# Kernel tuning notes

Hardware: AMD Instinct MI355X
Metric: run time of the kernel (lower is better)

The kernel has to match this reference:

```python
import jax, jax.numpy as jnp
import numpy as np

B, C_IN, S = 32, 4, 2048
NF = 256          # CNN filters
H = 256           # LSTM hidden per direction
NH, DH = 8, 64    # heads, single-head size
MH = 512          # multihead size
KSZ, PAD, POOL = 13, 6, 6
SP = (S + 2 * PAD - KSZ + 1) // POOL  # 341: post conv(len-preserving)+maxpool1d length


def _lstm_dir(x, Wih, Whh, b):
    # x: [T, N, C] -- torch LSTM gate order i,f,g,o; b = b_ih + b_hh merged
    N = x.shape[1]
    h0 = jnp.zeros((N, H), x.dtype)
    c0 = jnp.zeros((N, H), x.dtype)

    def step(carry, xt):
        h, c = carry
        g = xt @ Wih.T + h @ Whh.T + b
        i, f, gg, o = jnp.split(g, 4, axis=-1)
        c = jax.nn.sigmoid(f) * c + jax.nn.sigmoid(i) * jnp.tanh(gg)
        h = jax.nn.sigmoid(o) * jnp.tanh(c)
        return (h, c), h

    _, hs = jax.lax.scan(step, (h0, c0), x)
    return hs


def _bilstm(x, Wih, Whh, b):
    fwd = _lstm_dir(x, Wih[0], Whh[0], b[0])
    bwd = _lstm_dir(x[::-1], Wih[1], Whh[1], b[1])[::-1]
    return jnp.concatenate([fwd, bwd], axis=-1)


def _rpe():
    # RelativePosition: |clip(k-q, -(S-1), S-1)| / (S-1); identical across the
    # batch-repeat channels, so compute once then broadcast (same math).
    r = jnp.arange(S)
    d = jnp.abs(jnp.clip(r[None, :] - r[:, None], -(S - 1), S - 1))
    d = d.astype(jnp.float32) / jnp.float32(S - 1)
    # nn.MaxPool2d((9,9), stride=(6,6), padding=1) -> [341, 341]
    return jax.lax.reduce_window(d, -jnp.inf, jax.lax.max, (9, 9), (6, 6), [(1, 1), (1, 1)])


def setup_inputs():
    key = jax.random.key(0)
    ks = jax.random.split(key, 20)
    f = lambda i, shape: jax.random.normal(ks[i], shape, jnp.float32) * 0.05
    return {
        "inputs": jax.random.normal(ks[0], (B, C_IN, S), jnp.float32),
        "conv1_w": f(1, (NF, C_IN, KSZ)),
        "bn1_gamma": jnp.ones((NF,), jnp.float32),
        "bn1_beta": jnp.zeros((NF,), jnp.float32),
        "Wih0": f(2, (2, 4 * H, NF)),
        "Whh0": f(3, (2, 4 * H, H)),
        "b0": f(4, (2, 4 * H)),
        "Wih1": f(5, (2, 4 * H, 2 * H)),
        "Whh1": f(6, (2, 4 * H, H)),
        "b1": f(7, (2, 4 * H)),
        "Qw": f(8, (NH, DH, 2 * H)), "Qb": f(9, (NH, DH)),
        "Kw": f(10, (NH, DH, 2 * H)), "Kb": f(11, (NH, DH)),
        "Vw": f(12, (NH, DH, 2 * H)), "Vb": f(13, (NH, DH)),
        "mh_w": f(14, (MH, NH * DH)), "mh_b": f(15, (MH,)),
    }


def reference(inputs, conv1_w, bn1_gamma, bn1_beta, Wih0, Whh0, b0,
              Wih1, Whh1, b1, Qw, Qb, Kw, Kb, Vw, Vb, mh_w, mh_b):
    # layer1: Conv1d (bias=False, pad=6 keeps length) + BatchNorm1d(eval: mean=0, var=1) + ReLU + MaxPool1d(6)
    x = jax.lax.conv_general_dilated(inputs, conv1_w, (1,), [(PAD, PAD)],
                                     dimension_numbers=('NCH', 'OIH', 'NCH'))
    x = x * (bn1_gamma / jnp.sqrt(1.0 + 1e-5))[None, :, None] + bn1_beta[None, :, None]
    x = jax.nn.relu(x)
    x = jax.lax.reduce_window(x, -jnp.inf, jax.lax.max, (1, 1, POOL), (1, 1, POOL), 'VALID')  # [B,NF,SP]
    x = jnp.transpose(x, (0, 2, 1))  # [B, SP, NF]

    # torch nn.LSTM with batch_first=False fed [B,SP,NF]: scans over axis 0 (batch) -- replicated faithfully.
    x = _bilstm(x, Wih0, Whh0, b0)
    x = _bilstm(x, Wih1, Whh1, b1)  # [B, SP, 2H]
    # (the F_RNN/R_RNN split-and-concat is an identity)

    # per-head Q/K/V (batched over heads), relative attention, dropout off (eval)
    q = jnp.einsum('bsc,hdc->hbsd', x, Qw) + Qb[:, None, None, :]
    k = jnp.einsum('bsc,hdc->hbsd', x, Kw) + Kb[:, None, None, :]
    v = jnp.einsum('bsc,hdc->hbsd', x, Vw) + Vb[:, None, None, :]
    scores = jnp.einsum('hbqd,hbkd->hbqk', q, k) / jnp.sqrt(jnp.float32(DH))
    scores = scores / _rpe()[None, None, :, :]
    p = jax.nn.softmax(scores, axis=-1)
    attn = jax.nn.relu(jnp.einsum('hbqk,hbkd->hbqd', p, v))  # [NH,B,SP,DH]
    cat = jnp.transpose(attn, (1, 2, 0, 3)).reshape(B, SP, NH * DH)
    out = jax.nn.relu(cat @ mh_w.T + mh_b)  # MultiHeadLinear + MHReLU
    return out
```

## Files before the change

### kernel.cpp

```cpp
#include <hip/hip_runtime.h>
#include <math.h>

#define B_    32
#define CIN   4
#define SLEN  2048
#define NF    256
#define HD    256
#define SP    341
#define RTOT  (B_*SP)
#define NH_   8
#define DH_   64
#define GRP   4
#define PSTR  344
#define HS    (SP*HD)
#define PKS   768

typedef __attribute__((ext_vector_type(8))) short short8;
typedef __attribute__((ext_vector_type(4))) float floatx4;
typedef __attribute__((ext_vector_type(4))) unsigned short ushortx4;
typedef __attribute__((ext_vector_type(8))) unsigned short ushort8;

__device__ __forceinline__ float sigmoidf_(float x) { return 1.0f / (1.0f + expf(-x)); }

__device__ __forceinline__ unsigned short f2bf(float x) {
    unsigned int u = __float_as_uint(x);
    unsigned int r = (u + 0x7FFF + ((u >> 16) & 1)) >> 16;
    return (unsigned short)r;
}
__device__ __forceinline__ float bf2f(unsigned short b) {
    return __uint_as_float(((unsigned int)b) << 16);
}

__device__ __forceinline__ void store_f4_llc(float* p, floatx4 v)
{
    asm volatile("global_store_dwordx4 %0, %1, off sc0 sc1" :: "v"(p), "v"(v) : "memory");
}
__device__ __forceinline__ unsigned load_u32_llc(const unsigned* p)
{
    unsigned r;
    asm volatile("global_load_dword %0, %1, off sc0 sc1\n\ts_waitcnt vmcnt(0)"
                 : "=v"(r) : "v"(p) : "memory");
    return r;
}
__device__ __forceinline__ void load_h16_llc(const float* p, floatx4* r)
{
    asm volatile(
        "global_load_dwordx4 %0, %16, off sc0 sc1\n\t"
        "global_load_dwordx4 %1, %16, off offset:16 sc0 sc1\n\t"
        "global_load_dwordx4 %2, %16, off offset:128 sc0 sc1\n\t"
        "global_load_dwordx4 %3, %16, off offset:144 sc0 sc1\n\t"
        "global_load_dwordx4 %4, %16, off offset:256 sc0 sc1\n\t"
        "global_load_dwordx4 %5, %16, off offset:272 sc0 sc1\n\t"
        "global_load_dwordx4 %6, %16, off offset:384 sc0 sc1\n\t"
        "global_load_dwordx4 %7, %16, off offset:400 sc0 sc1\n\t"
        "global_load_dwordx4 %8, %16, off offset:512 sc0 sc1\n\t"
        "global_load_dwordx4 %9, %16, off offset:528 sc0 sc1\n\t"
        "global_load_dwordx4 %10, %16, off offset:640 sc0 sc1\n\t"
        "global_load_dwordx4 %11, %16, off offset:656 sc0 sc1\n\t"
        "global_load_dwordx4 %12, %16, off offset:768 sc0 sc1\n\t"
        "global_load_dwordx4 %13, %16, off offset:784 sc0 sc1\n\t"
        "global_load_dwordx4 %14, %16, off offset:896 sc0 sc1\n\t"
        "global_load_dwordx4 %15, %16, off offset:912 sc0 sc1\n\t"
        "s_waitcnt vmcnt(0)"
        : "=&v"(r[0]), "=&v"(r[1]), "=&v"(r[2]), "=&v"(r[3]),
          "=&v"(r[4]), "=&v"(r[5]), "=&v"(r[6]), "=&v"(r[7]),
          "=&v"(r[8]), "=&v"(r[9]), "=&v"(r[10]), "=&v"(r[11]),
          "=&v"(r[12]), "=&v"(r[13]), "=&v"(r[14]), "=&v"(r[15])
        : "v"(p)
        : "memory");
}


__global__ __launch_bounds__(256)
void conv_pool_k(const float* __restrict__ in, const float* __restrict__ cw,
                 const float* __restrict__ gamma, const float* __restrict__ beta,
                 unsigned short* __restrict__ x0p)
{
    const int b  = blockIdx.y;
    const int s0 = blockIdx.x * 16;
    const int co = threadIdx.x;
    __shared__ float ins[CIN][16*6 + 12];
    for (int idx = threadIdx.x; idx < CIN*108; idx += 256) {
        int ci = idx / 108, o = idx % 108;
        int pos = 6*s0 - 6 + o;
        ins[ci][o] = (pos >= 0 && pos < SLEN) ? in[(b*CIN + ci)*SLEN + pos] : 0.0f;
    }
    float wreg[52];
    {
        const float4* wp = (const float4*)(cw + co*52);
        #pragma unroll
        for (int j4 = 0; j4 < 13; ++j4) {
            float4 w4 = wp[j4];
            wreg[j4*4+0]=w4.x; wreg[j4*4+1]=w4.y; wreg[j4*4+2]=w4.z; wreg[j4*4+3]=w4.w;
        }
    }
    const float scale = gamma[co] * (1.0f / sqrtf(1.0f + 1e-5f));
    const float shift = beta[co];
    __syncthreads();
    for (int si = 0; si < 16; ++si) {
        int s = s0 + si;
        if (s >= SP) break;
        float win[CIN][18];
        #pragma unroll
        for (int ci = 0; ci < CIN; ++ci)
            #pragma unroll
            for (int o = 0; o < 18; ++o)
                win[ci][o] = ins[ci][6*si + o];
        float m = -1e30f;
        #pragma unroll
        for (int p6 = 0; p6 < 6; ++p6) {
            float acc = 0.0f;
            #pragma unroll
            for (int ci = 0; ci < CIN; ++ci)
                #pragma unroll
                for (int kk = 0; kk < 13; ++kk)
                    acc += win[ci][p6+kk] * wreg[ci*13+kk];
            float val = acc * scale + shift;
            val = fmaxf(val, 0.0f);
            m = fmaxf(m, val);
        }
        unsigned short hb_ = f2bf(m);
        unsigned short lb_ = f2bf(m - bf2f(hb_));
        size_t rb = (size_t)(b*SP + s)*512 + (size_t)(co >> 3)*16 + (co & 7);
        x0p[rb]     = hb_;
        x0p[rb + 8] = lb_;
    }
}

__global__ __launch_bounds__(256)
void pack4_k(const float* __restrict__ W, unsigned short* __restrict__ hi,
             unsigned short* __restrict__ lo, int n4)
{
    int i = blockIdx.x * 256 + threadIdx.x;
    if (i >= n4) return;
    float4 x = *((const float4*)W + i);
    float v[4] = {x.x, x.y, x.z, x.w};
    ushortx4 h, l;
    #pragma unroll
    for (int e = 0; e < 4; ++e) {
        unsigned short hb = f2bf(v[e]);
        h[e] = hb;
        l[e] = f2bf(v[e] - bf2f(hb));
    }
    *((ushortx4*)hi + i) = h;
    *((ushortx4*)lo + i) = l;
}

__global__ __launch_bounds__(256)
void pack8_k(const float* __restrict__ W, unsigned short* __restrict__ O, int n8)
{
    int i = blockIdx.x * 256 + threadIdx.x;
    if (i >= n8) return;
    const float4* wp = (const float4*)W + (size_t)i*2;
    float4 a = wp[0], b = wp[1];
    float v[8] = {a.x,a.y,a.z,a.w,b.x,b.y,b.z,b.w};
    ushort8 h, l;
    #pragma unroll
    for (int e = 0; e < 8; ++e) {
        unsigned short hb = f2bf(v[e]);
        h[e] = hb;
        l[e] = f2bf(v[e] - bf2f(hb));
    }
    *(ushort8*)(O + (size_t)i*16)     = h;
    *(ushort8*)(O + (size_t)i*16 + 8) = l;
}

template<int RELU>
__global__ __launch_bounds__(256)
void gemm_bf_k(const unsigned short* __restrict__ Ap, const unsigned short* __restrict__ Bp,
               const float* __restrict__ bias, float* __restrict__ C,
               int M, int N, int K)
{
    const int n0 = blockIdx.x * 128;
    const int m0 = blockIdx.y * 128;
    const int tid = threadIdx.x;
    const int lane = tid & 63;
    const int w = tid >> 6;
    const int wm = w >> 1, wn = w & 1;
    const int ln15 = lane & 15, lq = lane >> 4;
    const int l8 = lane >> 3, lj = lane & 7;
    const size_t rstr = 2*(size_t)K;

    __shared__ unsigned short As[128*64];
    __shared__ unsigned short Bs[128*64];

    floatx4 acc[4][4];
    #pragma unroll
    for (int i = 0; i < 4; ++i)
        #pragma unroll
        for (int j = 0; j < 4; ++j) acc[i][j] = (floatx4){0.f, 0.f, 0.f, 0.f};

    int rloc[4];
    #pragma unroll
    for (int c = 0; c < 4; ++c) rloc[c] = w*32 + c*8 + l8;
    const int spos = lj ^ (l8 & 7);

    for (int k0 = 0; k0 < K; k0 += 32) {
        short8 va[4], vb[4];
        #pragma unroll
        for (int c = 0; c < 4; ++c) {
            int gra = m0 + rloc[c]; if (gra >= M) gra = M - 1;
            va[c] = *(const short8*)(Ap + (size_t)gra*rstr + k0*2 + lj*8);
            vb[c] = *(const short8*)(Bp + (size_t)(n0 + rloc[c])*rstr + k0*2 + lj*8);
        }
        __syncthreads();
        #pragma unroll
        for (int c = 0; c < 4; ++c) {
            *(short8*)&As[rloc[c]*64 + spos*8] = va[c];
            *(short8*)&Bs[rloc[c]*64 + spos*8] = vb[c];
        }
        __syncthreads();

        short8 fa_h[4], fa_l[4], fb_h[4], fb_l[4];
        #pragma unroll
        for (int mt = 0; mt < 4; ++mt) {
            const int lr = wm*64 + mt*16 + ln15;
            fa_h[mt] = *(const short8*)&As[lr*64 + (((lq*2  ) ^ (lr&7))*8)];
            fa_l[mt] = *(const short8*)&As[lr*64 + (((lq*2+1) ^ (lr&7))*8)];
        }
        #pragma unroll
        for (int nt = 0; nt < 4; ++nt) {
            const int lr = wn*64 + nt*16 + ln15;
            fb_h[nt] = *(const short8*)&Bs[lr*64 + (((lq*2  ) ^ (lr&7))*8)];
            fb_l[nt] = *(const short8*)&Bs[lr*64 + (((lq*2+1) ^ (lr&7))*8)];
        }
        #pragma unroll
        for (int mt = 0; mt < 4; ++mt)
            #pragma unroll
            for (int nt = 0; nt < 4; ++nt) {
                acc[mt][nt] = __builtin_amdgcn_mfma_f32_16x16x32_bf16(fa_l[mt], fb_h[nt], acc[mt][nt], 0, 0, 0);
                acc[mt][nt] = __builtin_amdgcn_mfma_f32_16x16x32_bf16(fa_h[mt], fb_l[nt], acc[mt][nt], 0, 0, 0);
                acc[mt][nt] = __builtin_amdgcn_mfma_f32_16x16x32_bf16(fa_h[mt], fb_h[nt], acc[mt][nt], 0, 0, 0);
            }
    }

    #pragma unroll
    for (int nt = 0; nt < 4; ++nt) {
        const int n = n0 + wn*64 + nt*16 + ln15;
        const float bv = bias[n];
        #pragma unroll
        for (int mt = 0; mt < 4; ++mt) {
            const int mbase = m0 + wm*64 + mt*16 + lq*4;
            #pragma unroll
            for (int r = 0; r < 4; ++r) {
                int m = mbase + r;
                if (m < M) {
                    float val = acc[mt][nt][r] + bv;
                    if (RELU) val = fmaxf(val, 0.0f);
                    C[(size_t)m*N + n] = val;
                }
            }
        }
    }
}

__global__ __launch_bounds__(256)
void gemm_vT_k(const unsigned short* __restrict__ Ap, const unsigned short* __restrict__ Bp,
               const float* __restrict__ bias, unsigned short* __restrict__ vT,
               int M, int N, int K)
{
    const int n0 = blockIdx.x * 128;
    const int m0 = blockIdx.y * 128;
    const int tid = threadIdx.x;
    const int lane = tid & 63;
    const int w = tid >> 6;
    const int wm = w >> 1, wn = w & 1;
    const int ln15 = lane & 15, lq = lane >> 4;
    const int l8 = lane >> 3, lj = lane & 7;
    const size_t rstr = 2*(size_t)K;

    __shared__ unsigned short As[128*64];
    __shared__ unsigned short Bs[128*64];

    floatx4 acc[4][4];
    #pragma unroll
    for (int i = 0; i < 4; ++i)
        #pragma unroll
        for (int j = 0; j < 4; ++j) acc[i][j] = (floatx4){0.f, 0.f, 0.f, 0.f};

    int rloc[4];
    #pragma unroll
    for (int c = 0; c < 4; ++c) rloc[c] = w*32 + c*8 + l8;
    const int spos = lj ^ (l8 & 7);

    for (int k0 = 0; k0 < K; k0 += 32) {
        short8 va[4], vb[4];
        #pragma unroll
        for (int c = 0; c < 4; ++c) {
            int gra = m0 + rloc[c]; if (gra >= M) gra = M - 1;
            va[c] = *(const short8*)(Ap + (size_t)gra*rstr + k0*2 + lj*8);
            vb[c] = *(const short8*)(Bp + (size_t)(n0 + rloc[c])*rstr + k0*2 + lj*8);
        }
        __syncthreads();
        #pragma unroll
        for (int c = 0; c < 4; ++c) {
            *(short8*)&As[rloc[c]*64 + spos*8] = va[c];
            *(short8*)&Bs[rloc[c]*64 + spos*8] = vb[c];
        }
        __syncthreads();

        short8 fa_h[4], fa_l[4], fb_h[4], fb_l[4];
        #pragma unroll
        for (int mt = 0; mt < 4; ++mt) {
            const int lr = wm*64 + mt*16 + ln15;
            fa_h[mt] = *(const short8*)&As[lr*64 + (((lq*2  ) ^ (lr&7))*8)];
            fa_l[mt] = *(const short8*)&As[lr*64 + (((lq*2+1) ^ (lr&7))*8)];
        }
        #pragma unroll
        for (int nt = 0; nt < 4; ++nt) {
            const int lr = wn*64 + nt*16 + ln15;
            fb_h[nt] = *(const short8*)&Bs[lr*64 + (((lq*2  ) ^ (lr&7))*8)];
            fb_l[nt] = *(const short8*)&Bs[lr*64 + (((lq*2+1) ^ (lr&7))*8)];
        }
        #pragma unroll
        for (int mt = 0; mt < 4; ++mt)
            #pragma unroll
            for (int nt = 0; nt < 4; ++nt) {
                acc[mt][nt] = __builtin_amdgcn_mfma_f32_16x16x32_bf16(fa_l[mt], fb_h[nt], acc[mt][nt], 0, 0, 0);
                acc[mt][nt] = __builtin_amdgcn_mfma_f32_16x16x32_bf16(fa_h[mt], fb_l[nt], acc[mt][nt], 0, 0, 0);
                acc[mt][nt] = __builtin_amdgcn_mfma_f32_16x16x32_bf16(fa_h[mt], fb_h[nt], acc[mt][nt], 0, 0, 0);
            }
    }

    #pragma unroll
    for (int nt = 0; nt < 4; ++nt) {
        const int n = n0 + wn*64 + nt*16 + ln15;
        const float bv = bias[n];
        #pragma unroll
        for (int mt = 0; mt < 4; ++mt) {
            const int mbase = m0 + wm*64 + mt*16 + lq*4;
            #pragma unroll
            for (int r = 0; r < 4; ++r) {
                int m = mbase + r;
                if (m < M) {
                    float val = acc[mt][nt][r] + bv;
                    int bg = m / 341;
                    int sp = m - bg*341;
                    size_t vb_ = ((size_t)bg*512 + n)*PKS + (size_t)((sp >> 3)*16 + (sp & 7));
                    unsigned short hb16 = f2bf(val);
                    vT[vb_]     = hb16;
                    vT[vb_ + 8] = f2bf(val - bf2f(hb16));
                }
            }
        }
    }
}

__global__ __launch_bounds__(256)
void lstm_scan_k(const float* __restrict__ G,
                 const unsigned short* __restrict__ Whi,
                 const unsigned short* __restrict__ Wlo,
                 float* __restrict__ hb,
                 unsigned short* __restrict__ x_out,
                 unsigned* __restrict__ bar)
{
    const int j0 = blockIdx.x * 32;
    const int m0 = blockIdx.y * 32;
    const int d  = blockIdx.z;
    const int tid = threadIdx.x;
    const int w = tid >> 6, lane = tid & 63;
    const int mhalf = w & 1, gpair = w >> 1;
    const int ln15 = lane & 15, lq = lane >> 4;
    const size_t hsz = (size_t)2*SP*HD;
    unsigned* gbar = bar + (size_t)(blockIdx.y*2 + blockIdx.z)*64;

    __shared__ float Csh[32][132];

    int am = m0 + mhalf*16 + ln15; if (am > SP-1) am = SP-1;
    const int akoff = lq * 8;

    const unsigned short* WhiD = Whi + (size_t)d*1024*256;
    const unsigned short* WloD = Wlo + (size_t)d*1024*256;
    int nrow[4];
    #pragma unroll
    for (int t = 0; t < 4; ++t)
        nrow[t] = (gpair*2 + (t>>1))*256 + j0 + (t&1)*16 + ln15;

    const int emloc = tid >> 3;
    const int ej4   = (tid & 7) * 4;
    const int em    = m0 + emloc;

    floatx4 creg = (floatx4){0.f, 0.f, 0.f, 0.f};

    for (int s = 0; s < B_; ++s) {
        const int t_in = d ? (B_ - 1 - s) : s;
        float* hbuf_in  = hb + (size_t)(s & 1)*hsz;
        float* hbuf_out = hb + (size_t)((s+1) & 1)*hsz;

        floatx4 acc[4];
        #pragma unroll
        for (int t = 0; t < 4; ++t) acc[t] = (floatx4){0.f, 0.f, 0.f, 0.f};

        if (s > 0) {
            const float* p = hbuf_in + (size_t)d*HS + (size_t)am*HD + akoff;
            floatx4 hr[16];
            load_h16_llc(p, hr);
            #pragma unroll
            for (int kk = 0; kk < 8; ++kk) {
                const int ko = kk*32 + akoff;
                float vv[8] = {hr[2*kk][0], hr[2*kk][1], hr[2*kk][2], hr[2*kk][3],
                               hr[2*kk+1][0], hr[2*kk+1][1], hr[2*kk+1][2], hr[2*kk+1][3]};
                short8 ahi, alo;
                #pragma unroll
                for (int e = 0; e < 8; ++e) {
                    unsigned short hb16 = f2bf(vv[e]);
                    ahi[e] = (short)hb16;
                    alo[e] = (short)f2bf(vv[e] - bf2f(hb16));
                }
                #pragma unroll
                for (int t = 0; t < 4; ++t) {
                    short8 bhi = *(const short8*)(WhiD + (size_t)nrow[t]*HD + ko);
                    short8 blo = *(const short8*)(WloD + (size_t)nrow[t]*HD + ko);
                    acc[t] = __builtin_amdgcn_mfma_f32_16x16x32_bf16(alo, bhi, acc[t], 0, 0, 0);
                    acc[t] = __builtin_amdgcn_mfma_f32_16x16x32_bf16(ahi, blo, acc[t], 0, 0, 0);
                    acc[t] = __builtin_amdgcn_mfma_f32_16x16x32_bf16(ahi, bhi, acc[t], 0, 0, 0);
                }
            }
        }

        #pragma unroll
        for (int t = 0; t < 4; ++t) {
            int col = gpair*64 + (t>>1)*32 + (t&1)*16 + ln15;
            int rb  = mhalf*16 + lq*4;
            #pragma unroll
            for (int r = 0; r < 4; ++r)
                Csh[rb + r][col] = acc[t][r];
        }
        __syncthreads();

        if (em < SP) {
            size_t gb = ((size_t)t_in*SP + em)*2048 + (size_t)d*1024 + j0 + ej4;
            float4 gi4 = *(const float4*)&G[gb];
            float4 gf4 = *(const float4*)&G[gb + 256];
            float4 gg4 = *(const float4*)&G[gb + 512];
            float4 go4 = *(const float4*)&G[gb + 768];
            float hv[4];
            #pragma unroll
            for (int e = 0; e < 4; ++e) {
                float gi = Csh[emloc][     ej4+e] + (&gi4.x)[e];
                float gf = Csh[emloc][32 + ej4+e] + (&gf4.x)[e];
                float gg = Csh[emloc][64 + ej4+e] + (&gg4.x)[e];
                float go = Csh[emloc][96 + ej4+e] + (&go4.x)[e];
                float cn = sigmoidf_(gf)*creg[e] + sigmoidf_(gi)*tanhf(gg);
                creg[e] = cn;
                hv[e] = sigmoidf_(go)*tanhf(cn);
            }
            size_t cbase = ((size_t)d*SP + em)*HD + j0 + ej4;
            floatx4 ho = (floatx4){hv[0], hv[1], hv[2], hv[3]};
            store_f4_llc(&hbuf_out[cbase], ho);
            const int colg = d*HD + j0 + ej4;
            size_t xb = ((size_t)t_in*SP + em)*1024 + (size_t)(colg >> 3)*16 + (colg & 7);
            ushortx4 xh, xl;
            #pragma unroll
            for (int e = 0; e < 4; ++e) {
                unsigned short hb16 = f2bf(hv[e]);
                xh[e] = hb16;
                xl[e] = f2bf(hv[e] - bf2f(hb16));
            }
            *(ushortx4*)&x_out[xb]     = xh;
            *(ushortx4*)&x_out[xb + 8] = xl;
        }

        if (s < B_ - 1) {
            asm volatile("s_waitcnt vmcnt(0)" ::: "memory");
            __syncthreads();
            if (tid == 0) {
                atomicAdd(gbar, 1u);
                const unsigned target = (unsigned)(s + 1) * 8u;
                while (load_u32_llc(gbar) < target)
                    __builtin_amdgcn_s_sleep(2);
            }
            __syncthreads();
        }
    }
}

__global__ __launch_bounds__(256)
void scores_sm_k(const float* __restrict__ q, const float* __restrict__ k,
                 unsigned short* __restrict__ Ppk, int g)
{
    const int h = blockIdx.z, bl = blockIdx.y, bg = g*GRP + bl;
    const int q0 = blockIdx.x * 32;
    const int tid = threadIdx.x;
    const int tx = tid & 15, ty = tid >> 4;
    __shared__ float qs[32][68];
    __shared__ float ks[64][68];
    {
        int jr = tid >> 3, c8 = (tid & 7) * 8;
        int qq = q0 + jr; if (qq > SP-1) qq = SP-1;
        const float* qp = &q[((size_t)bg*SP + qq)*512 + h*64 + c8];
        *(float4*)&qs[jr][c8]     = *(const float4*)qp;
        *(float4*)&qs[jr][c8 + 4] = *(const float4*)(qp + 4);
    }
    float sv[2][24];
    for (int kc = 0; kc < 6; ++kc) {
        __syncthreads();
        {
            int jr = tid >> 2, c16 = (tid & 3) * 16;
            int kr = kc*64 + jr; if (kr > SP-1) kr = SP-1;
            const float* kp = &k[((size_t)bg*SP + kr)*512 + h*64 + c16];
            #pragma unroll
            for (int u = 0; u < 4; ++u)
                *(float4*)&ks[jr][c16 + u*4] = *(const float4*)(kp + u*4);
        }
        __syncthreads();
        float a_[2][4] = {{0.f,0.f,0.f,0.f},{0.f,0.f,0.f,0.f}};
        for (int d4 = 0; d4 < 64; d4 += 4) {
            float4 a0 = *(const float4*)&qs[ty][d4];
            float4 a1 = *(const float4*)&qs[ty + 16][d4];
            float4 b[4];
            #pragma unroll
            for (int j = 0; j < 4; ++j) b[j] = *(const float4*)&ks[tx + 16*j][d4];
            #pragma unroll
            for (int j = 0; j < 4; ++j) {
                a_[0][j] += a0.x*b[j].x + a0.y*b[j].y + a0.z*b[j].z + a0.w*b[j].w;
                a_[1][j] += a1.x*b[j].x + a1.y*b[j].y + a1.z*b[j].z + a1.w*b[j].w;
            }
        }
        #pragma unroll
        for (int i = 0; i < 2; ++i)
            #pragma unroll
            for (int j = 0; j < 4; ++j) sv[i][kc*4 + j] = a_[i][j];
    }
    #pragma unroll
    for (int i = 0; i < 2; ++i) {
        const int qq = q0 + ty + 16*i;
        int r0 = 6*qq - 1; if (r0 < 0) r0 = 0;
        int r1 = 6*qq + 7; if (r1 > SLEN-1) r1 = SLEN-1;
        float m = -1e30f;
        #pragma unroll
        for (int jj = 0; jj < 24; ++jj) {
            const int col = (jj >> 2)*64 + (jj & 3)*16 + tx;
            float s;
            if (col < SP) {
                int c0 = 6*col - 1; if (c0 < 0) c0 = 0;
                int c1 = 6*col + 7;
                int dd1 = c1 - r0; if (dd1 < 0) dd1 = -dd1;
                int dd2 = r1 - c0; if (dd2 < 0) dd2 = -dd2;
                int den = dd1 > dd2 ? dd1 : dd2;
                s = (sv[i][jj] * 0.125f) * 2047.0f / (float)den;
            } else s = -1e30f;
            sv[i][jj] = s;
            m = fmaxf(m, s);
        }
        #pragma unroll
        for (int o = 1; o < 16; o <<= 1) m = fmaxf(m, __shfl_xor(m, o, 64));
        float sum = 0.0f;
        #pragma unroll
        for (int jj = 0; jj < 24; ++jj) {
            float v = expf(sv[i][jj] - m);
            sv[i][jj] = v;
            sum += v;
        }
        #pragma unroll
        for (int o = 1; o < 16; o <<= 1) sum += __shfl_xor(sum, o, 64);
        const float inv = 1.0f / sum;
        if (qq < SP) {
            const size_t pb = ((size_t)(h*GRP + bl)*SP + qq) * PKS;
            #pragma unroll
            for (int jj = 0; jj < 24; ++jj) {
                const int col = (jj >> 2)*64 + (jj & 3)*16 + tx;
                float p = sv[i][jj] * inv;
                unsigned short hb16 = f2bf(p);
                size_t pp = pb + (size_t)((col >> 3)*16 + (col & 7));
                Ppk[pp]     = hb16;
                Ppk[pp + 8] = f2bf(p - bf2f(hb16));
            }
        }
    }
}

__global__ __launch_bounds__(256)
void pv_bf_k(const unsigned short* __restrict__ Ppk, const unsigned short* __restrict__ vT,
             unsigned short* __restrict__ catp, int g)
{
    const int h = blockIdx.z, bl = blockIdx.y, bg = g*GRP + bl;
    const int q0 = blockIdx.x * 64;
    const int tid = threadIdx.x;
    const int lane = tid & 63, w = tid >> 6;
    const int ln15 = lane & 15, lq = lane >> 4;
    const int l8 = lane >> 3, lj = lane & 7;
    __shared__ unsigned short As[64*64];
    __shared__ unsigned short Bs[64*64];
    floatx4 acc[4];
    #pragma unroll
    for (int nt = 0; nt < 4; ++nt) acc[nt] = (floatx4){0.f,0.f,0.f,0.f};
    const int spos = lj ^ (l8 & 7);
    const size_t prow = (size_t)(h*GRP + bl)*SP;
    const size_t vrow = (size_t)bg*512 + h*64;

    for (int step = 0; step < 12; ++step) {
        const int ku = step * 64;
        short8 va[2], vb[2];
        #pragma unroll
        for (int c = 0; c < 2; ++c) {
            const int r = w*16 + c*8 + l8;
            int qa = q0 + r; if (qa > SP-1) qa = SP-1;
            va[c] = *(const short8*)(Ppk + (prow + qa)*PKS + ku + lj*8);
            vb[c] = *(const short8*)(vT + (vrow + r)*PKS + ku + lj*8);
        }
        __syncthreads();
        #pragma unroll
        for (int c = 0; c < 2; ++c) {
            const int r = w*16 + c*8 + l8;
            *(short8*)&As[r*64 + spos*8] = va[c];
            *(short8*)&Bs[r*64 + spos*8] = vb[c];
        }
        __syncthreads();
        const int lrA = w*16 + ln15;
        short8 fa_h = *(const short8*)&As[lrA*64 + (((lq*2  ) ^ (lrA&7))*8)];
        short8 fa_l = *(const short8*)&As[lrA*64 + (((lq*2+1) ^ (lrA&7))*8)];
        #pragma unroll
        for (int nt = 0; nt < 4; ++nt) {
            const int lrB = nt*16 + ln15;
            short8 fb_h = *(const short8*)&Bs[lrB*64 + (((lq*2  ) ^ (lrB&7))*8)];
            short8 fb_l = *(const short8*)&Bs[lrB*64 + (((lq*2+1) ^ (lrB&7))*8)];
            acc[nt] = __builtin_amdgcn_mfma_f32_16x16x32_bf16(fa_l, fb_h, acc[nt], 0, 0, 0);
            acc[nt] = __builtin_amdgcn_mfma_f32_16x16x32_bf16(fa_h, fb_l, acc[nt], 0, 0, 0);
            acc[nt] = __builtin_amdgcn_mfma_f32_16x16x32_bf16(fa_h, fb_h, acc[nt], 0, 0, 0);
        }
    }
    #pragma unroll
    for (int nt = 0; nt < 4; ++nt) {
        const int colg = h*64 + nt*16 + ln15;
        #pragma unroll
        for (int r = 0; r < 4; ++r) {
            const int em = q0 + w*16 + lq*4 + r;
            if (em < SP) {
                float val = fmaxf(acc[nt][r], 0.0f);
                size_t xb = ((size_t)bg*SP + em)*1024 + (size_t)((colg >> 3)*16 + (colg & 7));
                unsigned short hb16 = f2bf(val);
                catp[xb]     = hb16;
                catp[xb + 8] = f2bf(val - bf2f(hb16));
            }
        }
    }
}

extern "C" void kernel_launch(void* const* d_in, const int* in_sizes, int n_in,
                              void* d_out, int out_size, void* d_ws, size_t ws_size,
                              hipStream_t stream)
{
    (void)in_sizes; (void)n_in; (void)out_size; (void)ws_size;
    const float* in    = (const float*)d_in[0];
    const float* cw    = (const float*)d_in[1];
    const float* gamma = (const float*)d_in[2];
    const float* beta  = (const float*)d_in[3];
    const float* Wih0  = (const float*)d_in[4];
    const float* Whh0  = (const float*)d_in[5];
    const float* b0    = (const float*)d_in[6];
    const float* Wih1  = (const float*)d_in[7];
    const float* Whh1  = (const float*)d_in[8];
    const float* b1    = (const float*)d_in[9];
    const float* Qw    = (const float*)d_in[10];
    const float* Qb    = (const float*)d_in[11];
    const float* Kw    = (const float*)d_in[12];
    const float* Kb    = (const float*)d_in[13];
    const float* Vw    = (const float*)d_in[14];
    const float* Vb    = (const float*)d_in[15];
    const float* mhw   = (const float*)d_in[16];
    const float* mhb   = (const float*)d_in[17];
    float* out = (float*)d_out;

    float* x0 = (float*)d_ws;
    float* G  = x0 + (size_t)RTOT*NF;
    float* x1 = G  + (size_t)RTOT*2048;
    float* x2 = x1 + (size_t)RTOT*512;
    float* hb = x2 + (size_t)RTOT*512;
    float* cb = hb + (size_t)2*2*SP*HD;

    float* qbuf = G;
    float* kbuf = G + (size_t)RTOT*512;
    unsigned short* vT  = (unsigned short*)(G + (size_t)2*RTOT*512);
    unsigned short* Ppk = (unsigned short*)(G + (size_t)2*RTOT*512 + 6291456);
    unsigned* bar = (unsigned*)cb;

    unsigned short* x0p = (unsigned short*)x0;
    unsigned short* whh1_hi = (unsigned short*)x0;
    unsigned short* whh1_lo = whh1_hi + (size_t)524288;
    unsigned short* qw_p = (unsigned short*)(x0 + (size_t)524288);
    unsigned short* kw_p = qw_p + (size_t)524288;
    unsigned short* vw_p = kw_p + (size_t)524288;
    unsigned short* mw_p = vw_p + (size_t)524288;
    unsigned short* wih0_p  = (unsigned short*)x2;
    unsigned short* wih1_p  = wih0_p + (size_t)1048576;
    unsigned short* whh0_hi = wih1_p + (size_t)2097152;
    unsigned short* whh0_lo = whh0_hi + (size_t)524288;
    unsigned short* x1p  = (unsigned short*)x1;
    unsigned short* catp = (unsigned short*)x1;
    unsigned short* x2p = (unsigned short*)x2;

    #define PACKGRID(n) dim3(((n) + 255) / 256)

    conv_pool_k<<<dim3(22, B_), 256, 0, stream>>>(in, cw, gamma, beta, x0p);
    pack8_k<<<PACKGRID(65536), 256, 0, stream>>>(Wih0, wih0_p, 65536);
    gemm_bf_k<0><<<dim3(16, 86), 256, 0, stream>>>(x0p, wih0_p, b0, G, RTOT, 2048, 256);
    pack4_k<<<PACKGRID(131072), 256, 0, stream>>>(Whh0, whh0_hi, whh0_lo, 131072);
    pack4_k<<<PACKGRID(131072), 256, 0, stream>>>(Whh1, whh1_hi, whh1_lo, 131072);
    pack8_k<<<PACKGRID(131072), 256, 0, stream>>>(Wih1, wih1_p, 131072);
    hipMemsetAsync(bar, 0, 22*64*sizeof(unsigned), stream);
    {
        const float* a0 = G; const unsigned short* a1 = whh0_hi; const unsigned short* a2 = whh0_lo;
        float* a3 = hb; unsigned short* a4 = x1p; unsigned* a5 = bar;
        void* kargs[] = {&a0, &a1, &a2, &a3, &a4, &a5};
        hipLaunchCooperativeKernel((void*)lstm_scan_k, dim3(8, 11, 2), dim3(256, 1, 1), kargs, 0, stream);
    }
    gemm_bf_k<0><<<dim3(16, 86), 256, 0, stream>>>(x1p, wih1_p, b1, G, RTOT, 2048, 512);
    hipMemsetAsync(bar, 0, 22*64*sizeof(unsigned), stream);
    {
        const float* a0 = G; const unsigned short* a1 = whh1_hi; const unsigned short* a2 = whh1_lo;
        float* a3 = hb; unsigned short* a4 = x2p; unsigned* a5 = bar;
        void* kargs[] = {&a0, &a1, &a2, &a3, &a4, &a5};
        hipLaunchCooperativeKernel((void*)lstm_scan_k, dim3(8, 11, 2), dim3(256, 1, 1), kargs, 0, stream);
    }
    pack8_k<<<PACKGRID(32768), 256, 0, stream>>>(Qw,  qw_p, 32768);
    pack8_k<<<PACKGRID(32768), 256, 0, stream>>>(Kw,  kw_p, 32768);
    pack8_k<<<PACKGRID(32768), 256, 0, stream>>>(Vw,  vw_p, 32768);
    pack8_k<<<PACKGRID(32768), 256, 0, stream>>>(mhw, mw_p, 32768);
    gemm_bf_k<0><<<dim3(4, 86), 256, 0, stream>>>(x2p, qw_p, Qb, qbuf, RTOT, 512, 512);
    gemm_bf_k<0><<<dim3(4, 86), 256, 0, stream>>>(x2p, kw_p, Kb, kbuf, RTOT, 512, 512);
    hipMemsetAsync(vT, 0, (size_t)B_*512*PKS*sizeof(unsigned short), stream);
    gemm_vT_k<<<dim3(4, 86), 256, 0, stream>>>(x2p, vw_p, Vb, vT, RTOT, 512, 512);
    for (int g = 0; g < B_/GRP; ++g) {
        scores_sm_k<<<dim3(11, GRP, NH_), 256, 0, stream>>>(qbuf, kbuf, Ppk, g);
        pv_bf_k    <<<dim3(6,  GRP, NH_), 256, 0, stream>>>(Ppk, vT, catp, g);
    }
    gemm_bf_k<1><<<dim3(4, 86), 256, 0, stream>>>(catp, mw_p, mhb, out, RTOT, 512, 512);
    #undef PACKGRID
}
```

Measured before the change: 1.699 ms.

## Drop transposed V GEMM; transpose and split V to bf16 inside PV kernel

The dedicated gemm_vT_k kernel, which wrote V transposed in packed hi/lo bf16 form, and its memset are removed. V is now produced by the generic GEMM as fp32 row-major, and pv_bf_k loads fp32 V, splits it into hi/lo bf16 and transposes it into padded shared memory on the fly. The PV loop now stages 128-wide K chunks with a padded stride instead of XOR swizzling. This removes a memset and scattered 2-byte global stores, at the cost of redundant conversion work in each PV block and possible LDS bank conflicts from the transposed scalar stores.

```diff
diff --git a/kernel.cpp b/kernel.cpp
--- a/kernel.cpp
+++ b/kernel.cpp
@@ -11,9 +11,9 @@
 #define NH_   8
 #define DH_   64
 #define GRP   4
-#define PSTR  344
 #define HS    (SP*HD)
 #define PKS   768
+#define BSTR  136
 
 typedef __attribute__((ext_vector_type(8))) short short8;
 typedef __attribute__((ext_vector_type(4))) float floatx4;
@@ -255,98 +255,6 @@
 }
 
 __global__ __launch_bounds__(256)
-void gemm_vT_k(const unsigned short* __restrict__ Ap, const unsigned short* __restrict__ Bp,
-               const float* __restrict__ bias, unsigned short* __restrict__ vT,
-               int M, int N, int K)
-{
-    const int n0 = blockIdx.x * 128;
-    const int m0 = blockIdx.y * 128;
-    const int tid = threadIdx.x;
-    const int lane = tid & 63;
-    const int w = tid >> 6;
-    const int wm = w >> 1, wn = w & 1;
-    const int ln15 = lane & 15, lq = lane >> 4;
-    const int l8 = lane >> 3, lj = lane & 7;
-    const size_t rstr = 2*(size_t)K;
-
-    __shared__ unsigned short As[128*64];
-    __shared__ unsigned short Bs[128*64];
-
-    floatx4 acc[4][4];
-    #pragma unroll
-    for (int i = 0; i < 4; ++i)
-        #pragma unroll
-        for (int j = 0; j < 4; ++j) acc[i][j] = (floatx4){0.f, 0.f, 0.f, 0.f};
-
-    int rloc[4];
-    #pragma unroll
-    for (int c = 0; c < 4; ++c) rloc[c] = w*32 + c*8 + l8;
-    const int spos = lj ^ (l8 & 7);
-
-    for (int k0 = 0; k0 < K; k0 += 32) {
-        short8 va[4], vb[4];
-        #pragma unroll
-        for (int c = 0; c < 4; ++c) {
-            int gra = m0 + rloc[c]; if (gra >= M) gra = M - 1;
-            va[c] = *(const short8*)(Ap + (size_t)gra*rstr + k0*2 + lj*8);
-            vb[c] = *(const short8*)(Bp + (size_t)(n0 + rloc[c])*rstr + k0*2 + lj*8);
-        }
-        __syncthreads();
-        #pragma unroll
-        for (int c = 0; c < 4; ++c) {
-            *(short8*)&As[rloc[c]*64 + spos*8] = va[c];
-            *(short8*)&Bs[rloc[c]*64 + spos*8] = vb[c];
-        }
-        __syncthreads();
-
-        short8 fa_h[4], fa_l[4], fb_h[4], fb_l[4];
-        #pragma unroll
-        for (int mt = 0; mt < 4; ++mt) {
-            const int lr = wm*64 + mt*16 + ln15;
-            fa_h[mt] = *(const short8*)&As[lr*64 + (((lq*2  ) ^ (lr&7))*8)];
-            fa_l[mt] = *(const short8*)&As[lr*64 + (((lq*2+1) ^ (lr&7))*8)];
-        }
-        #pragma unroll
-        for (int nt = 0; nt < 4; ++nt) {
-            const int lr = wn*64 + nt*16 + ln15;
-            fb_h[nt] = *(const short8*)&Bs[lr*64 + (((lq*2  ) ^ (lr&7))*8)];
-            fb_l[nt] = *(const short8*)&Bs[lr*64 + (((lq*2+1) ^ (lr&7))*8)];
-        }
-        #pragma unroll
-        for (int mt = 0; mt < 4; ++mt)
-            #pragma unroll
-            for (int nt = 0; nt < 4; ++nt) {
-                acc[mt][nt] = __builtin_amdgcn_mfma_f32_16x16x32_bf16(fa_l[mt], fb_h[nt], acc[mt][nt], 0, 0, 0);
-                acc[mt][nt] = __builtin_amdgcn_mfma_f32_16x16x32_bf16(fa_h[mt], fb_l[nt], acc[mt][nt], 0, 0, 0);
-                acc[mt][nt] = __builtin_amdgcn_mfma_f32_16x16x32_bf16(fa_h[mt], fb_h[nt], acc[mt][nt], 0, 0, 0);
-            }
-    }
-
-    #pragma unroll
-    for (int nt = 0; nt < 4; ++nt) {
-        const int n = n0 + wn*64 + nt*16 + ln15;
-        const float bv = bias[n];
-        #pragma unroll
-        for (int mt = 0; mt < 4; ++mt) {
-            const int mbase = m0 + wm*64 + mt*16 + lq*4;
-            #pragma unroll
-            for (int r = 0; r < 4; ++r) {
-                int m = mbase + r;
-                if (m < M) {
-                    float val = acc[mt][nt][r] + bv;
-                    int bg = m / 341;
-                    int sp = m - bg*341;
-                    size_t vb_ = ((size_t)bg*512 + n)*PKS + (size_t)((sp >> 3)*16 + (sp & 7));
-                    unsigned short hb16 = f2bf(val);
-                    vT[vb_]     = hb16;
-                    vT[vb_ + 8] = f2bf(val - bf2f(hb16));
-                }
-            }
-        }
-    }
-}
-
-__global__ __launch_bounds__(256)
 void lstm_scan_k(const float* __restrict__ G,
                  const unsigned short* __restrict__ Whi,
                  const unsigned short* __restrict__ Wlo,
@@ -571,7 +479,7 @@
 }
 
 __global__ __launch_bounds__(256)
-void pv_bf_k(const unsigned short* __restrict__ Ppk, const unsigned short* __restrict__ vT,
+void pv_bf_k(const unsigned short* __restrict__ Ppk, const float* __restrict__ vbuf,
              unsigned short* __restrict__ catp, int g)
 {
     const int h = blockIdx.z, bl = blockIdx.y, bg = g*GRP + bl;
@@ -579,45 +487,63 @@
     const int tid = threadIdx.x;
     const int lane = tid & 63, w = tid >> 6;
     const int ln15 = lane & 15, lq = lane >> 4;
-    const int l8 = lane >> 3, lj = lane & 7;
-    __shared__ unsigned short As[64*64];
-    __shared__ unsigned short Bs[64*64];
+    __shared__ unsigned short As[64][BSTR];
+    __shared__ unsigned short Bs[64][BSTR];
     floatx4 acc[4];
     #pragma unroll
     for (int nt = 0; nt < 4; ++nt) acc[nt] = (floatx4){0.f,0.f,0.f,0.f};
-    const int spos = lj ^ (l8 & 7);
     const size_t prow = (size_t)(h*GRP + bl)*SP;
-    const size_t vrow = (size_t)bg*512 + h*64;
-
-    for (int step = 0; step < 12; ++step) {
-        const int ku = step * 64;
-        short8 va[2], vb[2];
-        #pragma unroll
-        for (int c = 0; c < 2; ++c) {
-            const int r = w*16 + c*8 + l8;
-            int qa = q0 + r; if (qa > SP-1) qa = SP-1;
-            va[c] = *(const short8*)(Ppk + (prow + qa)*PKS + ku + lj*8);
-            vb[c] = *(const short8*)(vT + (vrow + r)*PKS + ku + lj*8);
+    const int sr = tid >> 2;
+    const int sa = (tid & 3) * 32;
+    const int sd = (tid & 3) * 16;
+
+    for (int chunk = 0; chunk < 6; ++chunk) {
+        int qa = q0 + sr; if (qa > SP-1) qa = SP-1;
+        const unsigned short* ap = Ppk + (prow + qa)*PKS + chunk*128 + sa;
+        short8 a0 = *(const short8*)ap;
+        short8 a1 = *(const short8*)(ap + 8);
+        short8 a2 = *(const short8*)(ap + 16);
+        short8 a3 = *(const short8*)(ap + 24);
+        const int kr = chunk*64 + sr;
+        float vv[16];
+        if (kr < SP) {
+            const float* vp = &vbuf[((size_t)bg*SP + kr)*512 + h*64 + sd];
+            *(float4*)&vv[0]  = ((const float4*)vp)[0];
+            *(float4*)&vv[4]  = ((const float4*)vp)[1];
+            *(float4*)&vv[8]  = ((const float4*)vp)[2];
+            *(float4*)&vv[12] = ((const float4*)vp)[3];
+        } else {
+            #pragma unroll
+            for (int e = 0; e < 16; ++e) vv[e] = 0.0f;
         }
         __syncthreads();
-        #pragma unroll
-        for (int c = 0; c < 2; ++c) {
-            const int r = w*16 + c*8 + l8;
-            *(short8*)&As[r*64 + spos*8] = va[c];
-            *(short8*)&Bs[r*64 + spos*8] = vb[c];
+        *(short8*)&As[sr][sa]      = a0;
+        *(short8*)&As[sr][sa + 8]  = a1;
+        *(short8*)&As[sr][sa + 16] = a2;
+        *(short8*)&As[sr][sa + 24] = a3;
+        {
+            const int c = (sr >> 3)*16 + (sr & 7);
+            #pragma unroll
+            for (int e = 0; e < 16; ++e) {
+                unsigned short hb16 = f2bf(vv[e]);
+                Bs[sd + e][c]     = hb16;
+                Bs[sd + e][c + 8] = f2bf(vv[e] - bf2f(hb16));
+            }
         }
         __syncthreads();
-        const int lrA = w*16 + ln15;
-        short8 fa_h = *(const short8*)&As[lrA*64 + (((lq*2  ) ^ (lrA&7))*8)];
-        short8 fa_l = *(const short8*)&As[lrA*64 + (((lq*2+1) ^ (lrA&7))*8)];
-        #pragma unroll
-        for (int nt = 0; nt < 4; ++nt) {
-            const int lrB = nt*16 + ln15;
-            short8 fb_h = *(const short8*)&Bs[lrB*64 + (((lq*2  ) ^ (lrB&7))*8)];
-            short8 fb_l = *(const short8*)&Bs[lrB*64 + (((lq*2+1) ^ (lrB&7))*8)];
-            acc[nt] = __builtin_amdgcn_mfma_f32_16x16x32_bf16(fa_l, fb_h, acc[nt], 0, 0, 0);
-            acc[nt] = __builtin_amdgcn_mfma_f32_16x16x32_bf16(fa_h, fb_l, acc[nt], 0, 0, 0);
-            acc[nt] = __builtin_amdgcn_mfma_f32_16x16x32_bf16(fa_h, fb_h, acc[nt], 0, 0, 0);
+        #pragma unroll
+        for (int s = 0; s < 2; ++s) {
+            const int ko = s*64 + lq*16;
+            short8 fa_h = *(const short8*)&As[w*16 + ln15][ko];
+            short8 fa_l = *(const short8*)&As[w*16 + ln15][ko + 8];
+            #pragma unroll
+            for (int nt = 0; nt < 4; ++nt) {
+                short8 fb_h = *(const short8*)&Bs[nt*16 + ln15][ko];
+                short8 fb_l = *(const short8*)&Bs[nt*16 + ln15][ko + 8];
+                acc[nt] = __builtin_amdgcn_mfma_f32_16x16x32_bf16(fa_l, fb_h, acc[nt], 0, 0, 0);
+                acc[nt] = __builtin_amdgcn_mfma_f32_16x16x32_bf16(fa_h, fb_l, acc[nt], 0, 0, 0);
+                acc[nt] = __builtin_amdgcn_mfma_f32_16x16x32_bf16(fa_h, fb_h, acc[nt], 0, 0, 0);
+            }
         }
     }
     #pragma unroll
@@ -671,8 +597,8 @@
 
     float* qbuf = G;
     float* kbuf = G + (size_t)RTOT*512;
-    unsigned short* vT  = (unsigned short*)(G + (size_t)2*RTOT*512);
-    unsigned short* Ppk = (unsigned short*)(G + (size_t)2*RTOT*512 + 6291456);
+    float* vbuf = G + (size_t)2*RTOT*512;
+    unsigned short* Ppk = (unsigned short*)(G + (size_t)3*RTOT*512);
     unsigned* bar = (unsigned*)cb;
 
     unsigned short* x0p = (unsigned short*)x0;
@@ -719,11 +645,10 @@
     pack8_k<<<PACKGRID(32768), 256, 0, stream>>>(mhw, mw_p, 32768);
     gemm_bf_k<0><<<dim3(4, 86), 256, 0, stream>>>(x2p, qw_p, Qb, qbuf, RTOT, 512, 512);
     gemm_bf_k<0><<<dim3(4, 86), 256, 0, stream>>>(x2p, kw_p, Kb, kbuf, RTOT, 512, 512);
-    hipMemsetAsync(vT, 0, (size_t)B_*512*PKS*sizeof(unsigned short), stream);
-    gemm_vT_k<<<dim3(4, 86), 256, 0, stream>>>(x2p, vw_p, Vb, vT, RTOT, 512, 512);
+    gemm_bf_k<0><<<dim3(4, 86), 256, 0, stream>>>(x2p, vw_p, Vb, vbuf, RTOT, 512, 512);
     for (int g = 0; g < B_/GRP; ++g) {
         scores_sm_k<<<dim3(11, GRP, NH_), 256, 0, stream>>>(qbuf, kbuf, Ppk, g);
-        pv_bf_k    <<<dim3(6,  GRP, NH_), 256, 0, stream>>>(Ppk, vT, catp, g);
+        pv_bf_k    <<<dim3(6,  GRP, NH_), 256, 0, stream>>>(Ppk, vbuf, catp, g);
     }
     gemm_bf_k<1><<<dim3(4, 86), 256, 0, stream>>>(catp, mw_p, mhb, out, RTOT, 512, 512);
     #undef PACKGRID
```

New measurement: 1.697 ms. About the same (-0.1%).
